# Kernel optimization log

Hardware: AMD Instinct MI355X
Metric: run time of the kernel (lower is better)

Reference implementation:

```python
import jax, jax.numpy as jnp
import numpy as np

BATCH = 512
SEQ = 500          # number of time points; SEQ-1 spline pieces
INPUT_CH = 8       # input (control) channels
HIDDEN = 64        # hidden channels (size of z)
HH = 128           # hidden_hidden channels of the CDE func MLP
OUT = 1            # output channels


def setup_inputs() -> dict:
    key = jax.random.key(0)
    ks = jax.random.split(key, 12)
    shp = (BATCH, SEQ - 1, INPUT_CH)
    times = jnp.linspace(0.0, 1.0, SEQ, dtype=jnp.float32)
    coeff_a = jax.random.normal(ks[0], shp, dtype=jnp.float32)
    coeff_b = jax.random.normal(ks[1], shp, dtype=jnp.float32)
    coeff_two_c = jax.random.normal(ks[2], shp, dtype=jnp.float32)
    coeff_three_d = jax.random.normal(ks[3], shp, dtype=jnp.float32)
    # learned parameters
    init_W = jax.random.normal(ks[4], (INPUT_CH, HIDDEN), dtype=jnp.float32) / np.sqrt(INPUT_CH)
    init_b = jnp.zeros((HIDDEN,), dtype=jnp.float32)
    f_W1 = jax.random.normal(ks[5], (HIDDEN, HH), dtype=jnp.float32) / np.sqrt(HIDDEN)
    f_b1 = jnp.zeros((HH,), dtype=jnp.float32)
    f_W2 = jax.random.normal(ks[6], (HH, HIDDEN * INPUT_CH), dtype=jnp.float32) / np.sqrt(HH)
    f_b2 = jnp.zeros((HIDDEN * INPUT_CH,), dtype=jnp.float32)
    lin_W = jax.random.normal(ks[7], (HIDDEN, OUT), dtype=jnp.float32) / np.sqrt(HIDDEN)
    lin_b = jnp.zeros((OUT,), dtype=jnp.float32)
    return dict(times=times, coeff_a=coeff_a, coeff_b=coeff_b,
                coeff_two_c=coeff_two_c, coeff_three_d=coeff_three_d,
                init_W=init_W, init_b=init_b, f_W1=f_W1, f_b1=f_b1,
                f_W2=f_W2, f_b2=f_b2, lin_W=lin_W, lin_b=lin_b)


def reference(times, coeff_a, coeff_b, coeff_two_c, coeff_three_d,
              init_W, init_b, f_W1, f_b1, f_W2, f_b2, lin_W, lin_b):
    n_pieces = coeff_b.shape[1]

    def _interpret_t(t):
        idx = jnp.clip(jnp.sum(t > times) - 1, 0, n_pieces - 1)
        frac = t - times[idx]
        return frac, idx

    def spline_eval(t):  # NaturalCubicSpline.evaluate -> (B, INPUT_CH)
        frac, idx = _interpret_t(t)
        inner = 0.5 * coeff_two_c[:, idx] + coeff_three_d[:, idx] * frac / 3.0
        inner = coeff_b[:, idx] + inner * frac
        return coeff_a[:, idx] + inner * frac

    def dX_dt(t):  # NaturalCubicSpline.derivative -> (B, INPUT_CH)
        frac, idx = _interpret_t(t)
        inner = coeff_two_c[:, idx] + coeff_three_d[:, idx] * frac
        return coeff_b[:, idx] + inner * frac

    def f(z):  # CDE vector field MLP -> (B, HIDDEN, INPUT_CH)
        h = jax.nn.relu(z @ f_W1 + f_b1)
        v = jnp.tanh(h @ f_W2 + f_b2)
        return v.reshape(z.shape[0], HIDDEN, INPUT_CH)

    def F(t, z):  # VectorField: f(z) @ dX/dt -> (B, HIDDEN)
        return jnp.einsum('bhi,bi->bh', f(z), dX_dt(t))

    # initial state from initial_network applied to X(t0)
    z0 = spline_eval(times[0]) @ init_W + init_b  # (B, HIDDEN)

    @jax.checkpoint
    def rk4_step(z, i):
        t0 = times[i]
        h = times[i + 1] - times[i]
        k1 = F(t0, z)
        k2 = F(t0 + 0.5 * h, z + 0.5 * h * k1)
        k3 = F(t0 + 0.5 * h, z + 0.5 * h * k2)
        k4 = F(t0 + h, z + h * k3)
        z_next = z + (h / 6.0) * (k1 + 2.0 * k2 + 2.0 * k3 + k4)
        return z_next, None

    zT, _ = jax.lax.scan(rk4_step, z0, jnp.arange(SEQ - 1))
    # final linear readout + sigmoid activation
    return jax.nn.sigmoid(zT @ lin_W + lin_b)  # (B, OUT)
```

## Files before the change

kernel.cpp:

```cpp
#include <hip/hip_runtime.h>

#define NPIECE 499
#define SEQN 500

typedef __attribute__((ext_vector_type(8))) short bf16x8;
typedef __attribute__((ext_vector_type(4))) float f32x4;

__device__ inline short f2bf(float x) {
    union { float f; unsigned u; } v; v.f = x;
    unsigned r = v.u + 0x7FFFu + ((v.u >> 16) & 1u);
    return (short)(r >> 16);
}

__device__ inline unsigned cvt_pk(float lo, float hi) {
    unsigned r;
    asm("v_cvt_pk_bf16_f32 %0, %1, %2" : "=v"(r) : "v"(lo), "v"(hi));
    return r;
}

__device__ inline float fast_tanh(float x) {
    float e = __builtin_amdgcn_exp2f(x * 2.8853900817779268f);
    float r = __builtin_amdgcn_rcpf(e + 1.0f);
    return fmaf(-2.0f, r, 1.0f);
}

__device__ inline float xor16(float x) {
    return __int_as_float(__builtin_amdgcn_ds_swizzle(__float_as_int(x), 0x401f));
}

__global__ void __launch_bounds__(512, 2)
cde_kernel(const float* __restrict__ times,
           const float* __restrict__ ca,  const float* __restrict__ cb,
           const float* __restrict__ c2c, const float* __restrict__ c3d,
           const float* __restrict__ initW, const float* __restrict__ initb,
           const float* __restrict__ W1,  const float* __restrict__ b1,
           const float* __restrict__ W2,  const float* __restrict__ b2,
           const float* __restrict__ linW, const float* __restrict__ linb,
           float* __restrict__ out)
{
    const int tid  = threadIdx.x;
    const int lane = tid & 63;
    const int wv   = tid >> 6;
    const int g    = lane >> 4;
    const int col  = lane & 15;
    const int g0   = g & 1, g1 = g >> 1;
    const int hi   = lane >> 5;
    const int s0   = blockIdx.x * 16;

    __shared__ __align__(16) float tl[SEQN];
    __shared__ __align__(16) short zflat[8][16][8];
    __shared__ __align__(16) short hflat[16][16][8];
    __shared__ __align__(16) float dxl[2][3][2][16][4];
    __shared__ __align__(16) float zinit[64][16];
    __shared__ __align__(16) float pred[8][16];

    for (int j = tid; j < SEQN; j += 512) tl[j] = times[j];

    bf16x8 a2[4][4];
    f32x4  b2f[4];
#pragma unroll
    for (int tt = 0; tt < 4; ++tt) {
        const int o = 16 * (4 * wv + tt) + col;
#pragma unroll
        for (int kk = 0; kk < 4; ++kk) {
            bf16x8 f;
#pragma unroll
            for (int e = 0; e < 8; ++e)
                f[e] = f2bf(W2[(32 * kk + 8 * g + e) * 512 + o]);
            a2[tt][kk] = f;
        }
#pragma unroll
        for (int r = 0; r < 4; ++r)
            b2f[tt][r] = b2[16 * (4 * wv + tt) + 4 * g + r];
    }
    bf16x8 a1[2];
    f32x4  b1f;
    {
        const int o = 16 * wv + col;
#pragma unroll
        for (int kk = 0; kk < 2; ++kk) {
            bf16x8 f;
#pragma unroll
            for (int e = 0; e < 8; ++e)
                f[e] = f2bf(W1[(32 * kk + 8 * g + e) * 128 + o]);
            a1[kk] = f;
        }
#pragma unroll
        for (int r = 0; r < 4; ++r) b1f[r] = b1[16 * wv + 4 * g + r];
    }

    __syncthreads();

#pragma unroll
    for (int v = 0; v < 2; ++v) {
        const int idx = tid * 2 + v, hid = idx >> 4, sm = idx & 15;
        float z = initb[hid];
#pragma unroll
        for (int c = 0; c < 8; ++c)
            z += ca[((size_t)(s0 + sm)) * (NPIECE * 8) + c] * initW[c * 64 + hid];
        zinit[hid][sm] = z;
        zflat[hid >> 3][sm][hid & 7] = f2bf(z);
    }
    const int pslot = tid >> 7, prr = tid & 127, psm = prr >> 3, pch = prr & 7;
    const size_t prow = ((size_t)(s0 + psm)) * (NPIECE * 8);
    if (tid < 384) {
        float t0n = tl[0], t1n = tl[1], hn = t1n - t0n; int p; float fr;
        if (pslot == 0)      { p = 0; fr = 0.0f; }
        else if (pslot == 1) { p = 0; fr = (t0n + 0.5f * hn) - t0n; }
        else { float t3 = t0n + hn;
               if (t3 > t1n) { p = 1; fr = t3 - t1n; } else { p = 0; fr = t3 - t0n; } }
        const size_t off = prow + (size_t)p * 8 + pch;
        dxl[0][pslot][pch >> 2][psm][pch & 3] = cb[off] + (c2c[off] + c3d[off] * fr) * fr;
    }
    __syncthreads();

    const bool owner = ((lane & 31) < 16);
    float zreg[4], zs[4];
#pragma unroll
    for (int tt = 0; tt < 4; ++tt) {
        zs[tt] = 0.f;
        zreg[tt] = zinit[8 * wv + 2 * tt + hi][col];
    }

    for (int i = 0; i < NPIECE; ++i) {
        const float hs = tl[i + 1] - tl[i];
        const float hs_half = 0.5f * hs, hs_sixth = hs * (1.0f / 6.0f);
        const int par = i & 1;

        float pb = 0.f, pc = 0.f, pd = 0.f, pfr = 0.f;
        const bool pf = (i + 1 < NPIECE) && (tid < 384);
        if (pf) {
            const int j = i + 1;
            float t0n = tl[j], t1n = tl[j + 1], hn = t1n - t0n; int p; float fr;
            if (pslot == 0)      { p = j - 1; fr = t0n - tl[j - 1]; }
            else if (pslot == 1) { p = j; fr = (t0n + 0.5f * hn) - t0n; }
            else { float t3 = t0n + hn;
                   if (j < NPIECE - 1 && t3 > t1n) { p = j + 1; fr = t3 - t1n; }
                   else                            { p = j;     fr = t3 - t0n; } }
            const size_t off = prow + (size_t)p * 8 + pch;
            pb = cb[off]; pc = c2c[off]; pd = c3d[off]; pfr = fr;
        }

#pragma unroll
        for (int st = 0; st < 4; ++st) {
            const int dsel = (st == 0) ? 0 : ((st == 3) ? 2 : 1);
            __syncthreads();

            if (st == 3 && pf)
                dxl[par ^ 1][pslot][pch >> 2][psm][pch & 3] = pb + (pc + pd * pfr) * pfr;

            bf16x8 bz0 = *(const bf16x8*)&zflat[g][col][0];
            bf16x8 bz1 = *(const bf16x8*)&zflat[4 + g][col][0];
            f32x4 ha;
            ha = __builtin_amdgcn_mfma_f32_16x16x32_bf16(a1[0], bz0, b1f, 0, 0, 0);
            ha = __builtin_amdgcn_mfma_f32_16x16x32_bf16(a1[1], bz1, ha, 0, 0, 0);
            int2 hw;
            hw.x = (int)cvt_pk(fmaxf(ha[0], 0.f), fmaxf(ha[1], 0.f));
            hw.y = (int)cvt_pk(fmaxf(ha[2], 0.f), fmaxf(ha[3], 0.f));
            *(int2*)&hflat[2 * wv + g1][col][4 * g0] = hw;
            __syncthreads();

            bf16x8 bh[4];
#pragma unroll
            for (int c = 0; c < 4; ++c)
                bh[c] = *(const bf16x8*)&hflat[4 * c + g][col][0];
            f32x4 cc[4];
#pragma unroll
            for (int tt = 0; tt < 4; ++tt)
                cc[tt] = __builtin_amdgcn_mfma_f32_16x16x32_bf16(a2[tt][0], bh[0], b2f[tt], 0, 0, 0);
#pragma unroll
            for (int kk = 1; kk < 4; ++kk)
#pragma unroll
                for (int tt = 0; tt < 4; ++tt)
                    cc[tt] = __builtin_amdgcn_mfma_f32_16x16x32_bf16(a2[tt][kk], bh[kk], cc[tt], 0, 0, 0);

            f32x4 dd = *(const f32x4*)&dxl[par][dsel][g0][col][0];
            float pt[4];
#pragma unroll
            for (int tt = 0; tt < 4; ++tt) {
                float sacc = 0.f;
#pragma unroll
                for (int r = 0; r < 4; ++r)
                    sacc = fmaf(fast_tanh(cc[tt][r]), dd[r], sacc);
                pt[tt] = sacc;
            }
#pragma unroll
            for (int tt = 0; tt < 4; ++tt)
                pt[tt] += xor16(pt[tt]);

            if (owner) {
#pragma unroll
                for (int tt = 0; tt < 4; ++tt) {
                    const float k = pt[tt];
                    float zst;
                    if (st == 0)      { zs[tt] = k;          zst = fmaf(hs_half, k, zreg[tt]); }
                    else if (st == 1) { zs[tt] = fmaf(2.f, k, zs[tt]); zst = fmaf(hs_half, k, zreg[tt]); }
                    else if (st == 2) { zs[tt] = fmaf(2.f, k, zs[tt]); zst = fmaf(hs, k, zreg[tt]); }
                    else              { zs[tt] += k;         zst = fmaf(hs_sixth, zs[tt], zreg[tt]);
                                        zreg[tt] = zst; }
                    zflat[wv][col][2 * tt + hi] = f2bf(zst);
                }
            }
        }
    }

    float p = 0.f;
#pragma unroll
    for (int tt = 0; tt < 4; ++tt) p += zreg[tt] * linW[8 * wv + 2 * tt + hi];
    p += __shfl_xor(p, 32);
    if (lane < 16) pred[wv][col] = p;
    __syncthreads();
    if (tid < 16) {
        float a = linb[0];
#pragma unroll
        for (int w = 0; w < 8; ++w) a += pred[w][tid];
        out[s0 + tid] = 1.0f / (1.0f + __expf(-a));
    }
}

extern "C" void kernel_launch(void* const* d_in, const int* in_sizes, int n_in,
                              void* d_out, int out_size, void* d_ws, size_t ws_size,
                              hipStream_t stream) {
    (void)in_sizes; (void)n_in; (void)d_ws; (void)ws_size; (void)out_size;
    const float* times = (const float*)d_in[0];
    const float* ca    = (const float*)d_in[1];
    const float* cb    = (const float*)d_in[2];
    const float* c2c   = (const float*)d_in[3];
    const float* c3d   = (const float*)d_in[4];
    const float* initW = (const float*)d_in[5];
    const float* initb = (const float*)d_in[6];
    const float* W1    = (const float*)d_in[7];
    const float* b1    = (const float*)d_in[8];
    const float* W2    = (const float*)d_in[9];
    const float* b2    = (const float*)d_in[10];
    const float* linW  = (const float*)d_in[11];
    const float* linb  = (const float*)d_in[12];
    cde_kernel<<<32, 512, 0, stream>>>(times, ca, cb, c2c, c3d, initW, initb,
                                       W1, b1, W2, b2, linW, linb, (float*)d_out);
}
```

Before: 1.866 ms.

## Swizzle LDS z/h layouts, pack z writes, hoist dX loads, pair tanh math

Applies an XOR swizzle to the column index of the zflat and hflat LDS buffers and permutes the W1 K-ordering, so each owner thread can write its four z values as one packed 8-byte store instead of four scalar bf16 stores. Row pointers are precomputed. The three dX/dt vectors are loaded once per step instead of once per stage. The tanh and dot-product arithmetic is rewritten over float2 vectors so packed FP32 instructions can be used. The aim is fewer LDS transactions and bank conflicts on the serial critical path; the risk is that the new layout and index permutation must match exactly, and the extra live registers may hurt occupancy.

Measured after the change: 1.870 ms. No clear change (+0.2%).

```diff
diff --git a/kernel.cpp b/kernel.cpp
--- a/kernel.cpp
+++ b/kernel.cpp
@@ -5,6 +5,7 @@
 
 typedef __attribute__((ext_vector_type(8))) short bf16x8;
 typedef __attribute__((ext_vector_type(4))) float f32x4;
+typedef __attribute__((ext_vector_type(2))) float f32x2;
 
 __device__ inline short f2bf(float x) {
     union { float f; unsigned u; } v; v.f = x;
@@ -16,12 +17,6 @@
     unsigned r;
     asm("v_cvt_pk_bf16_f32 %0, %1, %2" : "=v"(r) : "v"(lo), "v"(hi));
     return r;
-}
-
-__device__ inline float fast_tanh(float x) {
-    float e = __builtin_amdgcn_exp2f(x * 2.8853900817779268f);
-    float r = __builtin_amdgcn_rcpf(e + 1.0f);
-    return fmaf(-2.0f, r, 1.0f);
 }
 
 __device__ inline float xor16(float x) {
@@ -82,12 +77,22 @@
             bf16x8 f;
 #pragma unroll
             for (int e = 0; e < 8; ++e)
-                f[e] = f2bf(W1[(32 * kk + 8 * g + e) * 128 + o]);
+                f[e] = f2bf(W1[(32 * kk + 8 * g + 2 * (e & 3) + (e >> 2)) * 128 + o]);
             a1[kk] = f;
         }
 #pragma unroll
         for (int r = 0; r < 4; ++r) b1f[r] = b1[16 * wv + 4 * g + r];
     }
+
+    const int colz = col ^ (g & 3);
+    const short* zr0 = &zflat[g][colz][0];
+    const short* zr1 = &zflat[4 + g][colz][0];
+    const short* hr0 = &hflat[g][colz][0];
+    const short* hr1 = &hflat[4 + g][colz][0];
+    const short* hr2 = &hflat[8 + g][colz][0];
+    const short* hr3 = &hflat[12 + g][colz][0];
+    short* hwp = &hflat[2 * wv + g1][col ^ ((2 * wv + g1) & 3)][4 * g0];
+    short* zwp = &zflat[wv][col ^ (wv & 3)][4 * hi];
 
     __syncthreads();
 
@@ -99,7 +104,7 @@
         for (int c = 0; c < 8; ++c)
             z += ca[((size_t)(s0 + sm)) * (NPIECE * 8) + c] * initW[c * 64 + hid];
         zinit[hid][sm] = z;
-        zflat[hid >> 3][sm][hid & 7] = f2bf(z);
+        zflat[hid >> 3][sm ^ ((hid >> 3) & 3)][4 * (hid & 1) + ((hid & 7) >> 1)] = f2bf(z);
     }
     const int pslot = tid >> 7, prr = tid & 127, psm = prr >> 3, pch = prr & 7;
     const size_t prow = ((size_t)(s0 + psm)) * (NPIECE * 8);
@@ -141,65 +146,89 @@
             pb = cb[off]; pc = c2c[off]; pd = c3d[off]; pfr = fr;
         }
 
+        f32x4 ddr0, ddr1, ddr2;
 #pragma unroll
         for (int st = 0; st < 4; ++st) {
-            const int dsel = (st == 0) ? 0 : ((st == 3) ? 2 : 1);
             __syncthreads();
 
+            if (st == 0) {
+                ddr0 = *(const f32x4*)&dxl[par][0][g0][col][0];
+                ddr1 = *(const f32x4*)&dxl[par][1][g0][col][0];
+                ddr2 = *(const f32x4*)&dxl[par][2][g0][col][0];
+            }
             if (st == 3 && pf)
                 dxl[par ^ 1][pslot][pch >> 2][psm][pch & 3] = pb + (pc + pd * pfr) * pfr;
 
-            bf16x8 bz0 = *(const bf16x8*)&zflat[g][col][0];
-            bf16x8 bz1 = *(const bf16x8*)&zflat[4 + g][col][0];
+            bf16x8 bz0 = *(const bf16x8*)zr0;
+            bf16x8 bz1 = *(const bf16x8*)zr1;
             f32x4 ha;
             ha = __builtin_amdgcn_mfma_f32_16x16x32_bf16(a1[0], bz0, b1f, 0, 0, 0);
             ha = __builtin_amdgcn_mfma_f32_16x16x32_bf16(a1[1], bz1, ha, 0, 0, 0);
             int2 hw;
             hw.x = (int)cvt_pk(fmaxf(ha[0], 0.f), fmaxf(ha[1], 0.f));
             hw.y = (int)cvt_pk(fmaxf(ha[2], 0.f), fmaxf(ha[3], 0.f));
-            *(int2*)&hflat[2 * wv + g1][col][4 * g0] = hw;
+            *(int2*)hwp = hw;
             __syncthreads();
 
-            bf16x8 bh[4];
-#pragma unroll
-            for (int c = 0; c < 4; ++c)
-                bh[c] = *(const bf16x8*)&hflat[4 * c + g][col][0];
+            bf16x8 bh0 = *(const bf16x8*)hr0;
+            bf16x8 bh1 = *(const bf16x8*)hr1;
+            bf16x8 bh2 = *(const bf16x8*)hr2;
+            bf16x8 bh3 = *(const bf16x8*)hr3;
             f32x4 cc[4];
 #pragma unroll
             for (int tt = 0; tt < 4; ++tt)
-                cc[tt] = __builtin_amdgcn_mfma_f32_16x16x32_bf16(a2[tt][0], bh[0], b2f[tt], 0, 0, 0);
-#pragma unroll
-            for (int kk = 1; kk < 4; ++kk)
-#pragma unroll
-                for (int tt = 0; tt < 4; ++tt)
-                    cc[tt] = __builtin_amdgcn_mfma_f32_16x16x32_bf16(a2[tt][kk], bh[kk], cc[tt], 0, 0, 0);
-
-            f32x4 dd = *(const f32x4*)&dxl[par][dsel][g0][col][0];
+                cc[tt] = __builtin_amdgcn_mfma_f32_16x16x32_bf16(a2[tt][0], bh0, b2f[tt], 0, 0, 0);
+#pragma unroll
+            for (int tt = 0; tt < 4; ++tt)
+                cc[tt] = __builtin_amdgcn_mfma_f32_16x16x32_bf16(a2[tt][1], bh1, cc[tt], 0, 0, 0);
+#pragma unroll
+            for (int tt = 0; tt < 4; ++tt)
+                cc[tt] = __builtin_amdgcn_mfma_f32_16x16x32_bf16(a2[tt][2], bh2, cc[tt], 0, 0, 0);
+#pragma unroll
+            for (int tt = 0; tt < 4; ++tt)
+                cc[tt] = __builtin_amdgcn_mfma_f32_16x16x32_bf16(a2[tt][3], bh3, cc[tt], 0, 0, 0);
+
+            const f32x4 dd = (st == 0) ? ddr0 : ((st == 3) ? ddr2 : ddr1);
             float pt[4];
 #pragma unroll
             for (int tt = 0; tt < 4; ++tt) {
-                float sacc = 0.f;
-#pragma unroll
-                for (int r = 0; r < 4; ++r)
-                    sacc = fmaf(fast_tanh(cc[tt][r]), dd[r], sacc);
-                pt[tt] = sacc;
+                f32x2 s2 = {0.f, 0.f};
+#pragma unroll
+                for (int r2 = 0; r2 < 2; ++r2) {
+                    f32x2 x = { cc[tt][2 * r2], cc[tt][2 * r2 + 1] };
+                    f32x2 a = x * 2.8853900817779268f;
+                    f32x2 e = { __builtin_amdgcn_exp2f(a.x),
+                                __builtin_amdgcn_exp2f(a.y) };
+                    e = e + 1.0f;
+                    f32x2 rr = { __builtin_amdgcn_rcpf(e.x),
+                                 __builtin_amdgcn_rcpf(e.y) };
+                    f32x2 th = (-2.0f) * rr + 1.0f;
+                    f32x2 d2 = { dd[2 * r2], dd[2 * r2 + 1] };
+                    s2 = th * d2 + s2;
+                }
+                pt[tt] = s2.x + s2.y;
             }
 #pragma unroll
             for (int tt = 0; tt < 4; ++tt)
                 pt[tt] += xor16(pt[tt]);
 
             if (owner) {
+                float zw[4];
 #pragma unroll
                 for (int tt = 0; tt < 4; ++tt) {
                     const float k = pt[tt];
                     float zst;
-                    if (st == 0)      { zs[tt] = k;          zst = fmaf(hs_half, k, zreg[tt]); }
+                    if (st == 0)      { zs[tt] = k;                    zst = fmaf(hs_half, k, zreg[tt]); }
                     else if (st == 1) { zs[tt] = fmaf(2.f, k, zs[tt]); zst = fmaf(hs_half, k, zreg[tt]); }
                     else if (st == 2) { zs[tt] = fmaf(2.f, k, zs[tt]); zst = fmaf(hs, k, zreg[tt]); }
-                    else              { zs[tt] += k;         zst = fmaf(hs_sixth, zs[tt], zreg[tt]);
+                    else              { zs[tt] += k;                   zst = fmaf(hs_sixth, zs[tt], zreg[tt]);
                                         zreg[tt] = zst; }
-                    zflat[wv][col][2 * tt + hi] = f2bf(zst);
+                    zw[tt] = zst;
                 }
+                int2 wd;
+                wd.x = (int)cvt_pk(zw[0], zw[1]);
+                wd.y = (int)cvt_pk(zw[2], zw[3]);
+                *(int2*)zwp = wd;
             }
         }
     }
```
